# Kernel tuning notes

Measured on AMD Instinct MI355X. Metric: run time of the kernel, lower is better.

## Reference

```python
import jax, jax.numpy as jnp
import numpy as np

WS = 7
NUM_HEADS = 12
DIM = 384
HEAD_DIM = DIM // NUM_HEADS
SCALE = HEAD_DIM ** -0.5


def _rel_pos_index(ws: int) -> jnp.ndarray:
    coords = np.stack(np.meshgrid(np.arange(ws), np.arange(ws), indexing='ij'))  # (2, ws, ws)
    cf = coords.reshape(2, -1)                       # (2, ws*ws)
    rel = cf[:, :, None] - cf[:, None, :]            # (2, N, N)
    rel = rel.transpose(1, 2, 0).copy()              # (N, N, 2)
    rel[..., 0] += ws - 1
    rel[..., 1] += ws - 1
    rel[..., 0] *= 2 * ws - 1
    return jnp.asarray(rel.sum(-1))                  # (N, N) int indices into bias table


REL_IDX = _rel_pos_index(WS)


def setup_inputs() -> dict:
    key = jax.random.key(0)
    ks = jax.random.split(key, 7)
    BW, N, C = 4096, WS * WS, DIM
    num_win = 64
    return {
        'x': jax.random.normal(ks[0], (BW, N, C), jnp.float32),
        'mask': jax.random.normal(ks[1], (num_win, N, N), jnp.float32),
        'qkv_w': jax.random.normal(ks[2], (3 * C, C), jnp.float32) * 0.02,
        'qkv_b': jax.random.normal(ks[3], (3 * C,), jnp.float32) * 0.02,
        'proj_w': jax.random.normal(ks[4], (C, C), jnp.float32) * 0.02,
        'proj_b': jax.random.normal(ks[5], (C,), jnp.float32) * 0.02,
        'bias_table': jax.random.normal(ks[6], ((2 * WS - 1) ** 2, NUM_HEADS), jnp.float32) * 0.02,
    }


def reference(x, mask, qkv_w, qkv_b, proj_w, proj_b, bias_table):
    BW, N, C = x.shape
    H, hd = NUM_HEADS, HEAD_DIM
    # QKV projection: (BW, N, 3C) -> (3, BW, H, N, hd)
    qkv = (x @ qkv_w.T + qkv_b).reshape(BW, N, 3, H, hd).transpose(2, 0, 3, 1, 4)
    q, k, v = qkv[0], qkv[1], qkv[2]
    attn = jnp.einsum('bhnd,bhmd->bhnm', q, k) * SCALE  # (BW, H, N, N)
    bias = bias_table[REL_IDX]                          # (N, N, H)
    attn = attn + bias.transpose(2, 0, 1)[None]
    num_win = mask.shape[0]
    attn = attn.reshape(BW // num_win, num_win, H, N, N) + mask[None, :, None]
    attn = attn.reshape(BW, H, N, N)
    attn = jax.nn.softmax(attn, axis=-1)
    out = jnp.einsum('bhnm,bhmd->bhnd', attn, v)        # (BW, H, N, hd)
    out = out.transpose(0, 2, 1, 3).reshape(BW, N, C)
    return out @ proj_w.T + proj_b
```

## Files before the change

### kernel.cpp

```cpp
#include <hip/hip_runtime.h>

typedef unsigned short u16;
typedef unsigned int u32;
typedef __attribute__((ext_vector_type(8))) short short8;
typedef __attribute__((ext_vector_type(4))) float floatx4;

#define SCALE_Q 0.17677669529663687f

__device__ __forceinline__ u16 f2bf(float f) {
  u32 u = __float_as_uint(f);
  u = (u + 0x7fffu + ((u >> 16) & 1u)) >> 16;
  return (u16)u;
}

__device__ __forceinline__ void gload_lds16(const void* g, void* l) {
  __builtin_amdgcn_global_load_lds(
      (const __attribute__((address_space(1))) u32*)g,
      (__attribute__((address_space(3))) u32*)l, 16, 0, 0);
}

__device__ __forceinline__ floatx4 mfma16(short8 a, short8 b, floatx4 c) {
  return __builtin_amdgcn_mfma_f32_16x16x32_bf16(a, b, c, 0, 0, 0);
}

__global__ void cast_w_kernel(const float* __restrict__ qkv_w,
                              const float* __restrict__ proj_w,
                              u16* __restrict__ wb1, u16* __restrict__ wb2) {
  int idx = blockIdx.x * 256 + threadIdx.x;
  wb1[idx] = f2bf(qkv_w[idx]);
  if (idx < 147456) wb2[idx] = f2bf(proj_w[idx]);
}

__global__ void comb_kernel(const float* __restrict__ bias_table,
                            const float* __restrict__ mask,
                            float* __restrict__ comb) {
  int wh = blockIdx.x;
  int w = wh / 12, h = wh - w * 12;
  float* dst = comb + (size_t)wh * 4096;
  for (int e = threadIdx.x; e < 4096; e += 256) {
    int q = e >> 6, p = e & 63;
    float v;
    if (q >= 49) v = -1e30f;
    else if (p >= 49) v = 0.0f;
    else {
      int pi = p / 7, pj = p - pi * 7;
      int qi = q / 7, qj = q - qi * 7;
      int ridx = (pi - qi + 6) * 13 + (pj - qj + 6);
      v = bias_table[ridx * 12 + h] + mask[(size_t)w * 2401 + p * 49 + q];
    }
    dst[e] = v;
  }
}

__global__ __launch_bounds__(256) void qkv_gemm(const float* __restrict__ A,
                                                const u16* __restrict__ B,
                                                const float* __restrict__ bias,
                                                u16* __restrict__ C) {
  __shared__ u16 As[128 * 32];
  __shared__ u16 Bs[128 * 32];
  const int tid = threadIdx.x;
  const int lane = tid & 63;
  const int wave = tid >> 6;
  const int l15 = lane & 15;
  const int quad = lane >> 4;
  const int wr = wave >> 1, wc = wave & 1;
  const int tn = blockIdx.x % 9;
  const int tm = blockIdx.x / 9;

  floatx4 acc[4][4];
#pragma unroll
  for (int i = 0; i < 4; ++i)
#pragma unroll
    for (int j = 0; j < 4; ++j) acc[i][j] = (floatx4){0.f, 0.f, 0.f, 0.f};

  for (int kb = 0; kb < 12; ++kb) {
    const int k0 = kb * 32;
#pragma unroll
    for (int cc = 0; cc < 2; ++cc) {
      const int c = tid + cc * 256;
      const int m = c >> 2, kp = c & 3;
      const float* ap = A + (size_t)(tm * 128 + m) * 384 + k0 + kp * 8;
      const float4 f0 = *(const float4*)ap;
      const float4 f1 = *(const float4*)(ap + 4);
      uint4 pk;
      pk.x = (u32)f2bf(f0.x) | ((u32)f2bf(f0.y) << 16);
      pk.y = (u32)f2bf(f0.z) | ((u32)f2bf(f0.w) << 16);
      pk.z = (u32)f2bf(f1.x) | ((u32)f2bf(f1.y) << 16);
      pk.w = (u32)f2bf(f1.z) | ((u32)f2bf(f1.w) << 16);
      *(uint4*)(&As[c * 8]) = pk;
    }
#pragma unroll
    for (int r = 0; r < 2; ++r) {
      const int c = r * 256 + tid;
      const int n = c >> 2, kp = c & 3;
      gload_lds16(B + (size_t)(tn * 128 + n) * 384 + k0 + kp * 8, &Bs[c * 8]);
    }
    __syncthreads();
    short8 af[4], bfr[4];
#pragma unroll
    for (int i = 0; i < 4; ++i)
      af[i] = *(const short8*)(&As[(wr * 64 + i * 16 + l15) * 32 + quad * 8]);
#pragma unroll
    for (int i = 0; i < 4; ++i)
      bfr[i] = *(const short8*)(&Bs[(wc * 64 + i * 16 + l15) * 32 + quad * 8]);
#pragma unroll
    for (int mi = 0; mi < 4; ++mi)
#pragma unroll
      for (int ni = 0; ni < 4; ++ni)
        acc[mi][ni] = mfma16(af[mi], bfr[ni], acc[mi][ni]);
    __syncthreads();
  }
  const float scale = (tn < 3) ? SCALE_Q : 1.0f;
#pragma unroll
  for (int ni = 0; ni < 4; ++ni) {
    const int gcol = tn * 128 + wc * 64 + ni * 16 + l15;
    const float bb = bias[gcol];
#pragma unroll
    for (int mi = 0; mi < 4; ++mi) {
      const int grow0 = tm * 128 + wr * 64 + mi * 16 + quad * 4;
#pragma unroll
      for (int r = 0; r < 4; ++r)
        C[(size_t)(grow0 + r) * 1152 + gcol] = f2bf((acc[mi][ni][r] + bb) * scale);
    }
  }
}

__global__ __launch_bounds__(64) void attn_kernel(const u16* __restrict__ qkv,
                                                  const float* __restrict__ comb,
                                                  u16* __restrict__ ao) {
  __shared__ uint4 smem4[1184];
  char* smem = (char*)smem4;
  u16* Qs = (u16*)smem;
  u16* Ks = (u16*)(smem + 7168);
  u16* Vt = (u16*)(smem + 14336);
  u16* Ps = (u16*)smem;

  const int tid = threadIdx.x;
  const int l15 = tid & 15, quad = tid >> 4;
  const int bh = blockIdx.x;
  const int b = bh / 12, h = bh - b * 12;
  const int w = b & 63;

  const uint4 z = make_uint4(0u, 0u, 0u, 0u);
  for (int i = tid; i < 105; i += 64) smem4[343 + i] = z;
  for (int i = tid; i < 105; i += 64) smem4[791 + i] = z;
  for (int i = tid; i < 288; i += 64) smem4[896 + i] = z;
  __syncthreads();

  const size_t base = (size_t)b * 49 * 1152 + (size_t)h * 32;
  for (int s0 = tid; s0 < 196; s0 += 64) {
    const int t = s0 >> 2, part = s0 & 3;
    const u16* g = qkv + base + (size_t)t * 1152 + part * 8;
    const uint4 dq = *(const uint4*)(g);
    const uint4 dk = *(const uint4*)(g + 384);
    const uint4 dv = *(const uint4*)(g + 768);
    *(uint4*)(Qs + t * 56 + part * 8) = dq;
    *(uint4*)(Ks + t * 56 + part * 8) = dk;
    const int d0 = part * 8;
    const u32 vv[4] = {dv.x, dv.y, dv.z, dv.w};
#pragma unroll
    for (int j = 0; j < 4; ++j) {
      Vt[(d0 + 2 * j) * 72 + t] = (u16)(vv[j] & 0xffffu);
      Vt[(d0 + 2 * j + 1) * 72 + t] = (u16)(vv[j] >> 16);
    }
  }
  __syncthreads();

  short8 aq[4], bk[4];
#pragma unroll
  for (int i = 0; i < 4; ++i)
    aq[i] = *(const short8*)(Qs + (i * 16 + l15) * 56 + quad * 8);
#pragma unroll
  for (int i = 0; i < 4; ++i)
    bk[i] = *(const short8*)(Ks + (i * 16 + l15) * 56 + quad * 8);
  floatx4 s[4][4];
  const floatx4 z4 = (floatx4){0.f, 0.f, 0.f, 0.f};
#pragma unroll
  for (int mi = 0; mi < 4; ++mi)
#pragma unroll
    for (int ni = 0; ni < 4; ++ni) s[mi][ni] = mfma16(aq[mi], bk[ni], z4);

  const float* cb = comb + (size_t)(w * 12 + h) * 4096;
#pragma unroll
  for (int ni = 0; ni < 4; ++ni)
#pragma unroll
    for (int mi = 0; mi < 4; ++mi) {
      const float4 cv = *(const float4*)(cb + (ni * 16 + l15) * 64 + mi * 16 + quad * 4);
      s[mi][ni][0] += cv.x;
      s[mi][ni][1] += cv.y;
      s[mi][ni][2] += cv.z;
      s[mi][ni][3] += cv.w;
    }

  floatx4 mx[4], sm[4];
#pragma unroll
  for (int mi = 0; mi < 4; ++mi)
#pragma unroll
    for (int r = 0; r < 4; ++r) {
      float m0 = fmaxf(fmaxf(s[mi][0][r], s[mi][1][r]), fmaxf(s[mi][2][r], s[mi][3][r]));
      mx[mi][r] = m0;
    }
#pragma unroll
  for (int d = 1; d < 16; d <<= 1)
#pragma unroll
    for (int mi = 0; mi < 4; ++mi)
#pragma unroll
      for (int r = 0; r < 4; ++r)
        mx[mi][r] = fmaxf(mx[mi][r], __shfl_xor(mx[mi][r], d));
#pragma unroll
  for (int mi = 0; mi < 4; ++mi)
#pragma unroll
    for (int r = 0; r < 4; ++r) {
      float a = 0.f;
#pragma unroll
      for (int ni = 0; ni < 4; ++ni) {
        const float e = __expf(s[mi][ni][r] - mx[mi][r]);
        s[mi][ni][r] = e;
        a += e;
      }
      sm[mi][r] = a;
    }
#pragma unroll
  for (int d = 1; d < 16; d <<= 1)
#pragma unroll
    for (int mi = 0; mi < 4; ++mi)
#pragma unroll
      for (int r = 0; r < 4; ++r)
        sm[mi][r] += __shfl_xor(sm[mi][r], d);

  __syncthreads();
#pragma unroll
  for (int mi = 0; mi < 4; ++mi)
#pragma unroll
    for (int r = 0; r < 4; ++r) {
      const float rinv = 1.0f / sm[mi][r];
      const int row = mi * 16 + quad * 4 + r;
#pragma unroll
      for (int ni = 0; ni < 4; ++ni)
        Ps[row * 72 + ni * 16 + l15] = f2bf(s[mi][ni][r] * rinv);
    }
  __syncthreads();

  floatx4 o[4][2];
#pragma unroll
  for (int mi = 0; mi < 4; ++mi)
#pragma unroll
    for (int ni = 0; ni < 2; ++ni) o[mi][ni] = z4;
#pragma unroll
  for (int kk = 0; kk < 2; ++kk) {
    short8 ap[4], bv[2];
#pragma unroll
    for (int mi = 0; mi < 4; ++mi)
      ap[mi] = *(const short8*)(Ps + (mi * 16 + l15) * 72 + kk * 32 + quad * 8);
#pragma unroll
    for (int ni = 0; ni < 2; ++ni)
      bv[ni] = *(const short8*)(Vt + (ni * 16 + l15) * 72 + kk * 32 + quad * 8);
#pragma unroll
    for (int mi = 0; mi < 4; ++mi)
#pragma unroll
      for (int ni = 0; ni < 2; ++ni) o[mi][ni] = mfma16(ap[mi], bv[ni], o[mi][ni]);
  }
#pragma unroll
  for (int mi = 0; mi < 4; ++mi)
#pragma unroll
    for (int r = 0; r < 4; ++r) {
      const int row = mi * 16 + quad * 4 + r;
      if (row < 49) {
        u16* dst = ao + (size_t)(b * 49 + row) * 384 + h * 32;
#pragma unroll
        for (int ni = 0; ni < 2; ++ni)
          dst[ni * 16 + l15] = f2bf(o[mi][ni][r]);
      }
    }
}

__global__ __launch_bounds__(256) void proj_gemm(const u16* __restrict__ A,
                                                 const u16* __restrict__ B,
                                                 const float* __restrict__ bias,
                                                 float* __restrict__ C) {
  __shared__ u16 As[128 * 32];
  __shared__ u16 Bs[128 * 32];
  const int tid = threadIdx.x;
  const int lane = tid & 63;
  const int wave = tid >> 6;
  const int l15 = lane & 15;
  const int quad = lane >> 4;
  const int wr = wave >> 1, wc = wave & 1;
  const int tn = blockIdx.x % 3;
  const int tm = blockIdx.x / 3;

  floatx4 acc[4][4];
#pragma unroll
  for (int i = 0; i < 4; ++i)
#pragma unroll
    for (int j = 0; j < 4; ++j) acc[i][j] = (floatx4){0.f, 0.f, 0.f, 0.f};

  for (int kb = 0; kb < 12; ++kb) {
    const int k0 = kb * 32;
#pragma unroll
    for (int r = 0; r < 2; ++r) {
      const int c = r * 256 + tid;
      const int m = c >> 2, kp = c & 3;
      gload_lds16(A + (size_t)(tm * 128 + m) * 384 + k0 + kp * 8, &As[c * 8]);
      gload_lds16(B + (size_t)(tn * 128 + m) * 384 + k0 + kp * 8, &Bs[c * 8]);
    }
    __syncthreads();
    short8 af[4], bfr[4];
#pragma unroll
    for (int i = 0; i < 4; ++i)
      af[i] = *(const short8*)(&As[(wr * 64 + i * 16 + l15) * 32 + quad * 8]);
#pragma unroll
    for (int i = 0; i < 4; ++i)
      bfr[i] = *(const short8*)(&Bs[(wc * 64 + i * 16 + l15) * 32 + quad * 8]);
#pragma unroll
    for (int mi = 0; mi < 4; ++mi)
#pragma unroll
      for (int ni = 0; ni < 4; ++ni)
        acc[mi][ni] = mfma16(af[mi], bfr[ni], acc[mi][ni]);
    __syncthreads();
  }
#pragma unroll
  for (int ni = 0; ni < 4; ++ni) {
    const int gcol = tn * 128 + wc * 64 + ni * 16 + l15;
    const float bb = bias[gcol];
#pragma unroll
    for (int mi = 0; mi < 4; ++mi) {
      const int grow0 = tm * 128 + wr * 64 + mi * 16 + quad * 4;
#pragma unroll
      for (int r = 0; r < 4; ++r)
        C[(size_t)(grow0 + r) * 384 + gcol] = acc[mi][ni][r] + bb;
    }
  }
}

extern "C" void kernel_launch(void* const* d_in, const int* in_sizes, int n_in,
                              void* d_out, int out_size, void* d_ws, size_t ws_size,
                              hipStream_t stream) {
  const float* x = (const float*)d_in[0];
  const float* mask = (const float*)d_in[1];
  const float* qkv_w = (const float*)d_in[2];
  const float* qkv_b = (const float*)d_in[3];
  const float* proj_w = (const float*)d_in[4];
  const float* proj_b = (const float*)d_in[5];
  const float* bias_table = (const float*)d_in[6];
  float* out = (float*)d_out;
  char* ws = (char*)d_ws;

  u16* wb1 = (u16*)(ws);
  u16* wb2 = (u16*)(ws + 884736);
  float* comb = (float*)(ws + 1179648);
  u16* qkvb = (u16*)(ws + 13762560);
  u16* ao = (u16*)(ws + 476184576);

  hipLaunchKernelGGL(cast_w_kernel, dim3(1728), dim3(256), 0, stream, qkv_w, proj_w, wb1, wb2);
  hipLaunchKernelGGL(comb_kernel, dim3(768), dim3(256), 0, stream, bias_table, mask, comb);
  hipLaunchKernelGGL(qkv_gemm, dim3(14112), dim3(256), 0, stream, x, wb1, qkv_b, qkvb);
  hipLaunchKernelGGL(attn_kernel, dim3(49152), dim3(64), 0, stream, qkvb, comb, ao);
  hipLaunchKernelGGL(proj_gemm, dim3(4704), dim3(256), 0, stream, ao, wb2, proj_b, out);
}
```

Before: 1.289 ms.

## Pre-cast x to bf16, remap GEMM tiles per XCD, load Q/K directly to registers

Adds a separate kernel that casts x to bf16 once, so qkv_gemm no longer re-reads and converts fp32 A for each of its 9 N tiles and can fill LDS with direct global-to-LDS loads. Both GEMMs remap block IDs so that blocks sharing an M tile land on the same XCD, which is meant to improve L2 reuse. The attention kernel loads Q and K fragments straight from global memory into registers, skipping LDS staging and two barriers and shrinking shared memory for higher occupancy. The cost is an extra kernel launch plus a round trip for x in bf16, which reuses the ao buffer as scratch.

```diff
diff --git a/kernel.cpp b/kernel.cpp
--- a/kernel.cpp
+++ b/kernel.cpp
@@ -29,6 +29,19 @@
   int idx = blockIdx.x * 256 + threadIdx.x;
   wb1[idx] = f2bf(qkv_w[idx]);
   if (idx < 147456) wb2[idx] = f2bf(proj_w[idx]);
+}
+
+__global__ __launch_bounds__(256) void cast_x_kernel(const float* __restrict__ x,
+                                                     u16* __restrict__ xb) {
+  const size_t i = ((size_t)blockIdx.x * 256 + threadIdx.x) * 8;
+  const float4 f0 = *(const float4*)(x + i);
+  const float4 f1 = *(const float4*)(x + i + 4);
+  uint4 pk;
+  pk.x = (u32)f2bf(f0.x) | ((u32)f2bf(f0.y) << 16);
+  pk.y = (u32)f2bf(f0.z) | ((u32)f2bf(f0.w) << 16);
+  pk.z = (u32)f2bf(f1.x) | ((u32)f2bf(f1.y) << 16);
+  pk.w = (u32)f2bf(f1.z) | ((u32)f2bf(f1.w) << 16);
+  *(uint4*)(xb + i) = pk;
 }
 
 __global__ void comb_kernel(const float* __restrict__ bias_table,
@@ -52,7 +65,7 @@
   }
 }
 
-__global__ __launch_bounds__(256) void qkv_gemm(const float* __restrict__ A,
+__global__ __launch_bounds__(256) void qkv_gemm(const u16* __restrict__ A,
                                                 const u16* __restrict__ B,
                                                 const float* __restrict__ bias,
                                                 u16* __restrict__ C) {
@@ -64,8 +77,12 @@
   const int l15 = lane & 15;
   const int quad = lane >> 4;
   const int wr = wave >> 1, wc = wave & 1;
-  const int tn = blockIdx.x % 9;
-  const int tm = blockIdx.x / 9;
+  const u32 bid = blockIdx.x;
+  const u32 xcd = bid & 7;
+  const u32 slot = bid >> 3;
+  const u32 grp = slot / 9;
+  const u32 tn = slot - grp * 9;
+  const u32 tm = xcd * 196 + grp;
 
   floatx4 acc[4][4];
 #pragma unroll
@@ -76,24 +93,11 @@
   for (int kb = 0; kb < 12; ++kb) {
     const int k0 = kb * 32;
 #pragma unroll
-    for (int cc = 0; cc < 2; ++cc) {
-      const int c = tid + cc * 256;
-      const int m = c >> 2, kp = c & 3;
-      const float* ap = A + (size_t)(tm * 128 + m) * 384 + k0 + kp * 8;
-      const float4 f0 = *(const float4*)ap;
-      const float4 f1 = *(const float4*)(ap + 4);
-      uint4 pk;
-      pk.x = (u32)f2bf(f0.x) | ((u32)f2bf(f0.y) << 16);
-      pk.y = (u32)f2bf(f0.z) | ((u32)f2bf(f0.w) << 16);
-      pk.z = (u32)f2bf(f1.x) | ((u32)f2bf(f1.y) << 16);
-      pk.w = (u32)f2bf(f1.z) | ((u32)f2bf(f1.w) << 16);
-      *(uint4*)(&As[c * 8]) = pk;
-    }
-#pragma unroll
     for (int r = 0; r < 2; ++r) {
       const int c = r * 256 + tid;
-      const int n = c >> 2, kp = c & 3;
-      gload_lds16(B + (size_t)(tn * 128 + n) * 384 + k0 + kp * 8, &Bs[c * 8]);
+      const int m = c >> 2, kp = c & 3;
+      gload_lds16(A + (size_t)(tm * 128 + m) * 384 + k0 + kp * 8, &As[c * 8]);
+      gload_lds16(B + (size_t)(tn * 128 + m) * 384 + k0 + kp * 8, &Bs[c * 8]);
     }
     __syncthreads();
     short8 af[4], bfr[4];
@@ -128,12 +132,9 @@
 __global__ __launch_bounds__(64) void attn_kernel(const u16* __restrict__ qkv,
                                                   const float* __restrict__ comb,
                                                   u16* __restrict__ ao) {
-  __shared__ uint4 smem4[1184];
-  char* smem = (char*)smem4;
-  u16* Qs = (u16*)smem;
-  u16* Ks = (u16*)(smem + 7168);
-  u16* Vt = (u16*)(smem + 14336);
-  u16* Ps = (u16*)smem;
+  __shared__ uint4 smem4[864];
+  u16* Ps = (u16*)smem4;
+  u16* Vt = (u16*)((char*)smem4 + 9216);
 
   const int tid = threadIdx.x;
   const int l15 = tid & 15, quad = tid >> 4;
@@ -142,20 +143,13 @@
   const int w = b & 63;
 
   const uint4 z = make_uint4(0u, 0u, 0u, 0u);
-  for (int i = tid; i < 105; i += 64) smem4[343 + i] = z;
-  for (int i = tid; i < 105; i += 64) smem4[791 + i] = z;
-  for (int i = tid; i < 288; i += 64) smem4[896 + i] = z;
-  __syncthreads();
+  for (int i = tid; i < 288; i += 64) smem4[576 + i] = z;
 
   const size_t base = (size_t)b * 49 * 1152 + (size_t)h * 32;
+  const u16* vbase = qkv + base + 768;
   for (int s0 = tid; s0 < 196; s0 += 64) {
     const int t = s0 >> 2, part = s0 & 3;
-    const u16* g = qkv + base + (size_t)t * 1152 + part * 8;
-    const uint4 dq = *(const uint4*)(g);
-    const uint4 dk = *(const uint4*)(g + 384);
-    const uint4 dv = *(const uint4*)(g + 768);
-    *(uint4*)(Qs + t * 56 + part * 8) = dq;
-    *(uint4*)(Ks + t * 56 + part * 8) = dk;
+    const uint4 dv = *(const uint4*)(vbase + (size_t)t * 1152 + part * 8);
     const int d0 = part * 8;
     const u32 vv[4] = {dv.x, dv.y, dv.z, dv.w};
 #pragma unroll
@@ -164,15 +158,18 @@
       Vt[(d0 + 2 * j + 1) * 72 + t] = (u16)(vv[j] >> 16);
     }
   }
-  __syncthreads();
-
+
+  const u16* qbase = qkv + base + quad * 8;
   short8 aq[4], bk[4];
-#pragma unroll
-  for (int i = 0; i < 4; ++i)
-    aq[i] = *(const short8*)(Qs + (i * 16 + l15) * 56 + quad * 8);
-#pragma unroll
-  for (int i = 0; i < 4; ++i)
-    bk[i] = *(const short8*)(Ks + (i * 16 + l15) * 56 + quad * 8);
+  const short8 z8 = {0, 0, 0, 0, 0, 0, 0, 0};
+#pragma unroll
+  for (int i = 0; i < 3; ++i) {
+    aq[i] = *(const short8*)(qbase + (size_t)(i * 16 + l15) * 1152);
+    bk[i] = *(const short8*)(qbase + 384 + (size_t)(i * 16 + l15) * 1152);
+  }
+  aq[3] = (l15 == 0) ? *(const short8*)(qbase + (size_t)48 * 1152) : z8;
+  bk[3] = (l15 == 0) ? *(const short8*)(qbase + 384 + (size_t)48 * 1152) : z8;
+
   floatx4 s[4][4];
   const floatx4 z4 = (floatx4){0.f, 0.f, 0.f, 0.f};
 #pragma unroll
@@ -196,10 +193,8 @@
 #pragma unroll
   for (int mi = 0; mi < 4; ++mi)
 #pragma unroll
-    for (int r = 0; r < 4; ++r) {
-      float m0 = fmaxf(fmaxf(s[mi][0][r], s[mi][1][r]), fmaxf(s[mi][2][r], s[mi][3][r]));
-      mx[mi][r] = m0;
-    }
+    for (int r = 0; r < 4; ++r)
+      mx[mi][r] = fmaxf(fmaxf(s[mi][0][r], s[mi][1][r]), fmaxf(s[mi][2][r], s[mi][3][r]));
 #pragma unroll
   for (int d = 1; d < 16; d <<= 1)
 #pragma unroll
@@ -228,7 +223,6 @@
       for (int r = 0; r < 4; ++r)
         sm[mi][r] += __shfl_xor(sm[mi][r], d);
 
-  __syncthreads();
 #pragma unroll
   for (int mi = 0; mi < 4; ++mi)
 #pragma unroll
@@ -286,8 +280,12 @@
   const int l15 = lane & 15;
   const int quad = lane >> 4;
   const int wr = wave >> 1, wc = wave & 1;
-  const int tn = blockIdx.x % 3;
-  const int tm = blockIdx.x / 3;
+  const u32 bid = blockIdx.x;
+  const u32 xcd = bid & 7;
+  const u32 slot = bid >> 3;
+  const u32 grp = slot / 3;
+  const u32 tn = slot - grp * 3;
+  const u32 tm = xcd * 196 + grp;
 
   floatx4 acc[4][4];
 #pragma unroll
@@ -351,10 +349,12 @@
   float* comb = (float*)(ws + 1179648);
   u16* qkvb = (u16*)(ws + 13762560);
   u16* ao = (u16*)(ws + 476184576);
+  u16* xb = ao;
 
   hipLaunchKernelGGL(cast_w_kernel, dim3(1728), dim3(256), 0, stream, qkv_w, proj_w, wb1, wb2);
+  hipLaunchKernelGGL(cast_x_kernel, dim3(37632), dim3(256), 0, stream, x, xb);
   hipLaunchKernelGGL(comb_kernel, dim3(768), dim3(256), 0, stream, bias_table, mask, comb);
-  hipLaunchKernelGGL(qkv_gemm, dim3(14112), dim3(256), 0, stream, x, wb1, qkv_b, qkvb);
+  hipLaunchKernelGGL(qkv_gemm, dim3(14112), dim3(256), 0, stream, xb, wb1, qkv_b, qkvb);
   hipLaunchKernelGGL(attn_kernel, dim3(49152), dim3(64), 0, stream, qkvb, comb, ao);
   hipLaunchKernelGGL(proj_gemm, dim3(4704), dim3(256), 0, stream, ao, wb2, proj_b, out);
 }
```

After: 1.210 ms. 6.2% less time.
